# Kernel tuning notes

Measured on AMD Instinct MI355X. Metric: run time of the kernel, lower is better.

## Reference

```python
import jax, jax.numpy as jnp
import numpy as np

L1 = 1e-3  # init kwarg l1
EPS_NORM = 1e-12  # torch F.normalize eps


def _l2_normalize(x):
    # F.normalize(x, p=2, dim=1)
    n = jnp.linalg.norm(x, axis=1, keepdims=True)
    return x / jnp.maximum(n, EPS_NORM)


def _rbf_kernel(x):
    # x: [n, d]
    x2 = jnp.sum(x * x, axis=1, keepdims=True)          # [n,1]
    dist = x2 + x2.T - 2.0 * (x @ x.T)                   # [n,n]
    dist = jnp.maximum(dist, 0.0)
    # torch.median on even-size input returns the LOWER middle element
    flat = jnp.sort(jax.lax.stop_gradient(dist).ravel())
    median_dist = flat[(flat.shape[0] - 1) // 2]
    sigma2 = median_dist + 1e-5
    return jnp.exp(-dist / (2.0 * sigma2))


def _hsic(x, y):
    # x, y: [n, d]. Note: original normalizes in forward AND in hsic; L2
    # normalization is idempotent, so one normalize here is exact.
    x = _l2_normalize(x)
    y = _l2_normalize(y)
    K = _rbf_kernel(x)
    L = _rbf_kernel(y)
    n = K.shape[0]
    # K @ H with H = I - 1/n  ==  K - row_mean(K)
    KH = K - jnp.mean(K, axis=1, keepdims=True)
    LH = L - jnp.mean(L, axis=1, keepdims=True)
    return jnp.sum(KH * LH.T) / float((n - 1) ** 2)


def setup_inputs() -> dict:
    key = jax.random.key(0)
    k1, k2, k3, k4 = jax.random.split(key, 4)
    N, D = 65536, 512     # patches, feature dim
    K_INST, NS = 256, 32  # instances, samples per instance (== max_bg_samples)
    dp = jax.random.normal(k1, (N, D), dtype=jnp.float32)
    gate = jax.random.normal(k2, (N, D), dtype=jnp.float32)
    inst_idx = jax.random.randint(k3, (K_INST, NS), 0, N, dtype=jnp.int64)
    bg_idx = jax.random.randint(k4, (K_INST, NS), 0, N, dtype=jnp.int64)
    return {"dp": dp, "gate": gate, "inst_idx": inst_idx, "bg_idx": bg_idx}


def reference(dp, gate, inst_idx, bg_idx):
    x = dp[inst_idx]   # [K, n, d] per-instance foreground samples
    bg = dp[bg_idx]    # [K, n, d] per-instance background samples
    hs = jax.vmap(_hsic)(x, bg)  # [K]
    return jnp.mean(hs) + L1 * jnp.mean(jnp.abs(gate))
```

## Files before the change

### kernel.cpp

```cpp
#include <hip/hip_runtime.h>
#include <hip/hip_bf16.h>

#define NS 32
#define FD 512
#define K_INST 256
#define CHUNK 256
#define C4 (CHUNK/4)
#define PADF 260
#define PAD4 (PADF/4)
#define MPAD 33
#define HSIC_BLOCKS 512
#define GATE_BLOCKS 512
#define GATE_ITERS 64
#define GATE_N4 (65536*512/4)

__device__ __forceinline__ float wave_reduce_add(float v) {
  for (int off = 32; off; off >>= 1) v += __shfl_down(v, off, 64);
  return v;
}

__global__ __launch_bounds__(256) void fused_kernel(
    const float* __restrict__ dp, const float* __restrict__ gate,
    const int* __restrict__ inst_idx, const int* __restrict__ bg_idx,
    float* __restrict__ ws_gate, float* __restrict__ ws_mats,
    float* __restrict__ ws_means) {

  __shared__ float sX[NS * PADF];
  __shared__ float sD[NS * MPAD];
  __shared__ float sRowM[NS];
  __shared__ float sInv[NS];
  __shared__ float sN2[NS];
  __shared__ int   sIdx[NS];
  __shared__ int   sHist[256];
  __shared__ int   sWaveSum[4];
  __shared__ float sWaveRed[4];
  __shared__ unsigned sPrefix;
  __shared__ int   sWant;

  const int tid  = threadIdx.x;
  const int bid  = blockIdx.x;
  const int lane = tid & 63;
  const int w    = tid >> 6;

  if (bid >= HSIC_BLOCKS) {
    const int gb = bid - HSIC_BLOCKS;
    const float4* g4 = reinterpret_cast<const float4*>(gate);
    float s = 0.f;
    size_t base = (size_t)gb * 256 + tid;
    #pragma unroll 8
    for (int it = 0; it < GATE_ITERS; ++it) {
      float4 v = g4[base + (size_t)it * (GATE_BLOCKS * 256)];
      s += fabsf(v.x) + fabsf(v.y) + fabsf(v.z) + fabsf(v.w);
    }
    s = wave_reduce_add(s);
    if (lane == 0) sWaveRed[w] = s;
    __syncthreads();
    if (tid == 0) ws_gate[gb] = sWaveRed[0] + sWaveRed[1] + sWaveRed[2] + sWaveRed[3];
    return;
  }

  const int k = bid >> 1;
  const int m = bid & 1;
  const int ti = tid >> 4;
  const int tj = tid & 15;
  const float4* sX4 = reinterpret_cast<const float4*>(sX);

  const int* idx = (m == 0 ? inst_idx : bg_idx) + k * NS;
  if (tid < NS) sIdx[tid] = idx[tid];
  __syncthreads();

  float a00 = 0.f, a01 = 0.f, a10 = 0.f, a11 = 0.f;
  for (int ch = 0; ch < 2; ++ch) {
    for (int q = tid; q < NS * C4; q += 256) {
      int r = q >> 6, c = q & 63;
      float4 v = *(reinterpret_cast<const float4*>(dp + (size_t)sIdx[r] * FD + ch * CHUNK) + c);
      *(reinterpret_cast<float4*>(&sX[r * PADF]) + c) = v;
    }
    __syncthreads();
    #pragma unroll 4
    for (int c = 0; c < C4; ++c) {
      float4 x0 = sX4[ti * PAD4 + c];
      float4 x1 = sX4[(ti + 16) * PAD4 + c];
      float4 y0 = sX4[tj * PAD4 + c];
      float4 y1 = sX4[(tj + 16) * PAD4 + c];
      a00 += x0.x*y0.x + x0.y*y0.y + x0.z*y0.z + x0.w*y0.w;
      a01 += x0.x*y1.x + x0.y*y1.y + x0.z*y1.z + x0.w*y1.w;
      a10 += x1.x*y0.x + x1.y*y0.y + x1.z*y0.z + x1.w*y0.w;
      a11 += x1.x*y1.x + x1.y*y1.y + x1.z*y1.z + x1.w*y1.w;
    }
    __syncthreads();
  }

  if (ti == tj) { sN2[ti] = a00; sN2[ti + 16] = a11; }
  __syncthreads();
  if (tid < NS) sInv[tid] = 1.f / fmaxf(sqrtf(sN2[tid]), 1e-12f);
  __syncthreads();

  {
    float i0 = sInv[ti], i1 = sInv[ti + 16], j0 = sInv[tj], j1 = sInv[tj + 16];
    sD[ti * MPAD + tj]               = (ti == tj) ? 0.f : fmaxf(2.f - 2.f * a00 * i0 * j0, 0.f);
    sD[ti * MPAD + (tj + 16)]        = fmaxf(2.f - 2.f * a01 * i0 * j1, 0.f);
    sD[(ti + 16) * MPAD + tj]        = fmaxf(2.f - 2.f * a10 * i1 * j0, 0.f);
    sD[(ti + 16) * MPAD + (tj + 16)] = (ti == tj) ? 0.f : fmaxf(2.f - 2.f * a11 * i1 * j1, 0.f);
  }
  if (tid == 0) { sPrefix = 0u; sWant = (NS * NS - 1) / 2; }
  __syncthreads();

  for (int shift = 24; shift >= 0; shift -= 8) {
    sHist[tid] = 0;
    __syncthreads();
    unsigned pref = sPrefix;
    int want = sWant;
    unsigned hi_mask = (shift == 24) ? 0u : (0xFFFFFFFFu << (shift + 8));
    for (int q = tid; q < NS * NS; q += 256) {
      unsigned u = __float_as_uint(sD[(q >> 5) * MPAD + (q & 31)]);
      if ((u & hi_mask) == pref) atomicAdd(&sHist[(u >> shift) & 255], 1);
    }
    __syncthreads();
    int v = sHist[tid];
    int x = v;
    for (int off = 1; off < 64; off <<= 1) {
      int y = __shfl_up(x, off, 64);
      if (lane >= off) x += y;
    }
    if (lane == 63) sWaveSum[w] = x;
    __syncthreads();
    int add = 0;
    for (int ww = 0; ww < w; ++ww) add += sWaveSum[ww];
    x += add;
    int ex = x - v;
    if (ex <= want && want < ex + v) {
      sPrefix = pref | ((unsigned)tid << shift);
      sWant   = want - ex;
    }
    __syncthreads();
  }
  float sigma2 = __uint_as_float(sPrefix) + 1e-5f;

  float inv2s = -1.f / (2.f * sigma2);
  for (int q = tid; q < NS * NS; q += 256) {
    int i = q >> 5, j = q & 31;
    sD[i * MPAD + j] = expf(sD[i * MPAD + j] * inv2s);
  }
  __syncthreads();

  {
    int r = tid >> 3, g = tid & 7;
    float p = 0.f;
    #pragma unroll
    for (int s = 0; s < 4; ++s) p += sD[r * MPAD + g + 8 * s];
    for (int off = 4; off; off >>= 1) p += __shfl_down(p, off, 8);
    if (g == 0) sRowM[r] = p * (1.f / 32.f);
  }
  __syncthreads();

  float* mat = ws_mats + (size_t)bid * 1024;
  for (int q = tid; q < NS * NS; q += 256)
    mat[q] = sD[(q >> 5) * MPAD + (q & 31)];
  if (tid < NS) ws_means[bid * NS + tid] = sRowM[tid];
}

__global__ __launch_bounds__(256) void contract_kernel(
    const float* __restrict__ ws_mats, const float* __restrict__ ws_means,
    float* __restrict__ ws_hs) {
  __shared__ float sRM[2][NS];
  __shared__ float sWaveRed[4];
  const int k = blockIdx.x;
  const int tid = threadIdx.x, lane = tid & 63, w = tid >> 6;
  const float* Km = ws_mats + (size_t)(k * 2 + 0) * 1024;
  const float* Lm = ws_mats + (size_t)(k * 2 + 1) * 1024;
  if (tid < 64) sRM[tid >> 5][tid & 31] = ws_means[(k * 2 + (tid >> 5)) * NS + (tid & 31)];
  __syncthreads();
  float part = 0.f;
  for (int q = tid; q < NS * NS; q += 256) {
    int i = q >> 5, j = q & 31;
    part += (Km[q] - sRM[0][i]) * (Lm[q] - sRM[1][j]);
  }
  part = wave_reduce_add(part);
  if (lane == 0) sWaveRed[w] = part;
  __syncthreads();
  if (tid == 0)
    ws_hs[k] = (sWaveRed[0] + sWaveRed[1] + sWaveRed[2] + sWaveRed[3]) * (1.f / 961.f);
}

__global__ __launch_bounds__(256) void final_kernel(
    const float* __restrict__ ws_gate, const float* __restrict__ ws_hs,
    float* __restrict__ out) {
  __shared__ float sW[8];
  const int tid = threadIdx.x, lane = tid & 63, wave = tid >> 6;
  float g = 0.f;
  for (int i = tid; i < GATE_BLOCKS; i += 256) g += ws_gate[i];
  g = wave_reduce_add(g);
  if (lane == 0) sW[wave] = g;
  float h = (tid < K_INST) ? ws_hs[tid] : 0.f;
  h = wave_reduce_add(h);
  if (lane == 0) sW[4 + wave] = h;
  __syncthreads();
  if (tid == 0) {
    float gsum = sW[0] + sW[1] + sW[2] + sW[3];
    float hsum = sW[4] + sW[5] + sW[6] + sW[7];
    out[0] = hsum * (1.f / 256.f) + 1e-3f * (gsum / (65536.f * 512.f));
  }
}

extern "C" void kernel_launch(void* const* d_in, const int* in_sizes, int n_in,
                              void* d_out, int out_size, void* d_ws, size_t ws_size,
                              hipStream_t stream) {
  const float* dp   = (const float*)d_in[0];
  const float* gate = (const float*)d_in[1];
  const int*   inst = (const int*)d_in[2];
  const int*   bg   = (const int*)d_in[3];
  float* out = (float*)d_out;
  float* ws  = (float*)d_ws;
  float* ws_gate  = ws;
  float* ws_hs    = ws + 1024;
  float* ws_means = ws + 1024 + 256;
  float* ws_mats  = ws + 1024 + 256 + 512 * 32;

  fused_kernel<<<HSIC_BLOCKS + GATE_BLOCKS, 256, 0, stream>>>(
      dp, gate, inst, bg, ws_gate, ws_mats, ws_means);
  contract_kernel<<<K_INST, 256, 0, stream>>>(ws_mats, ws_means, ws_hs);
  final_kernel<<<1, 256, 0, stream>>>(ws_gate, ws_hs, out);
}
```

Baseline: 45.71 us.

## Keep distance matrix in registers, aggregate histogram atomics, split gate work finer

Each thread now keeps its four distance values in registers instead of writing them to a shared-memory matrix. The norms, exp, row means and output writes are computed directly from those registers, which removes several __syncthreads barriers and LDS round trips. The first radix-select pass aggregates atomics per bin across the wave using ballot, and the histogram is reset inline. The gate reduction is spread over twice as many blocks with half the iterations each, which adds more blocks in exchange for better load balance.

After: 47.68 us. 4.3% more time.

```diff
diff --git a/kernel.cpp b/kernel.cpp
--- a/kernel.cpp
+++ b/kernel.cpp
@@ -8,11 +8,9 @@
 #define C4 (CHUNK/4)
 #define PADF 260
 #define PAD4 (PADF/4)
-#define MPAD 33
 #define HSIC_BLOCKS 512
-#define GATE_BLOCKS 512
-#define GATE_ITERS 64
-#define GATE_N4 (65536*512/4)
+#define GATE_BLOCKS 1024
+#define GATE_ITERS 32
 
 __device__ __forceinline__ float wave_reduce_add(float v) {
   for (int off = 32; off; off >>= 1) v += __shfl_down(v, off, 64);
@@ -26,9 +24,6 @@
     float* __restrict__ ws_means) {
 
   __shared__ float sX[NS * PADF];
-  __shared__ float sD[NS * MPAD];
-  __shared__ float sRowM[NS];
-  __shared__ float sInv[NS];
   __shared__ float sN2[NS];
   __shared__ int   sIdx[NS];
   __shared__ int   sHist[256];
@@ -59,14 +54,16 @@
     return;
   }
 
-  const int k = bid >> 1;
-  const int m = bid & 1;
+  const int k  = bid >> 1;
+  const int m  = bid & 1;
   const int ti = tid >> 4;
   const int tj = tid & 15;
   const float4* sX4 = reinterpret_cast<const float4*>(sX);
 
   const int* idx = (m == 0 ? inst_idx : bg_idx) + k * NS;
   if (tid < NS) sIdx[tid] = idx[tid];
+  sHist[tid] = 0;
+  if (tid == 0) { sPrefix = 0u; sWant = (NS * NS - 1) / 2; }
   __syncthreads();
 
   float a00 = 0.f, a01 = 0.f, a10 = 0.f, a11 = 0.f;
@@ -93,31 +90,44 @@
 
   if (ti == tj) { sN2[ti] = a00; sN2[ti + 16] = a11; }
   __syncthreads();
-  if (tid < NS) sInv[tid] = 1.f / fmaxf(sqrtf(sN2[tid]), 1e-12f);
-  __syncthreads();
-
-  {
-    float i0 = sInv[ti], i1 = sInv[ti + 16], j0 = sInv[tj], j1 = sInv[tj + 16];
-    sD[ti * MPAD + tj]               = (ti == tj) ? 0.f : fmaxf(2.f - 2.f * a00 * i0 * j0, 0.f);
-    sD[ti * MPAD + (tj + 16)]        = fmaxf(2.f - 2.f * a01 * i0 * j1, 0.f);
-    sD[(ti + 16) * MPAD + tj]        = fmaxf(2.f - 2.f * a10 * i1 * j0, 0.f);
-    sD[(ti + 16) * MPAD + (tj + 16)] = (ti == tj) ? 0.f : fmaxf(2.f - 2.f * a11 * i1 * j1, 0.f);
-  }
-  if (tid == 0) { sPrefix = 0u; sWant = (NS * NS - 1) / 2; }
-  __syncthreads();
-
+  float i0 = 1.f / fmaxf(sqrtf(sN2[ti]),      1e-12f);
+  float i1 = 1.f / fmaxf(sqrtf(sN2[ti + 16]), 1e-12f);
+  float j0 = 1.f / fmaxf(sqrtf(sN2[tj]),      1e-12f);
+  float j1 = 1.f / fmaxf(sqrtf(sN2[tj + 16]), 1e-12f);
+
+  float d0 = (ti == tj) ? 0.f : fmaxf(2.f - 2.f * a00 * i0 * j0, 0.f);
+  float d1 = fmaxf(2.f - 2.f * a01 * i0 * j1, 0.f);
+  float d2 = fmaxf(2.f - 2.f * a10 * i1 * j0, 0.f);
+  float d3 = (ti == tj) ? 0.f : fmaxf(2.f - 2.f * a11 * i1 * j1, 0.f);
+  unsigned u[4] = { __float_as_uint(d0), __float_as_uint(d1),
+                    __float_as_uint(d2), __float_as_uint(d3) };
+
+  #pragma unroll 1
   for (int shift = 24; shift >= 0; shift -= 8) {
-    sHist[tid] = 0;
-    __syncthreads();
     unsigned pref = sPrefix;
     int want = sWant;
-    unsigned hi_mask = (shift == 24) ? 0u : (0xFFFFFFFFu << (shift + 8));
-    for (int q = tid; q < NS * NS; q += 256) {
-      unsigned u = __float_as_uint(sD[(q >> 5) * MPAD + (q & 31)]);
-      if ((u & hi_mask) == pref) atomicAdd(&sHist[(u >> shift) & 255], 1);
+    if (shift == 24) {
+      #pragma unroll
+      for (int s = 0; s < 4; ++s) {
+        int bin = (int)(u[s] >> 24);
+        unsigned long long act = __ballot(1);
+        while (act) {
+          int leader = (int)__builtin_ctzll(act);
+          int lbin = __shfl(bin, leader, 64);
+          unsigned long long mm = __ballot(bin == lbin);
+          if (lane == leader) atomicAdd(&sHist[lbin], (int)__popcll(mm));
+          act &= ~mm;
+        }
+      }
+    } else {
+      unsigned hi_mask = 0xFFFFFFFFu << (shift + 8);
+      #pragma unroll
+      for (int s = 0; s < 4; ++s)
+        if ((u[s] & hi_mask) == pref) atomicAdd(&sHist[(u[s] >> shift) & 255], 1);
     }
     __syncthreads();
     int v = sHist[tid];
+    sHist[tid] = 0;
     int x = v;
     for (int off = 1; off < 64; off <<= 1) {
       int y = __shfl_up(x, off, 64);
@@ -138,26 +148,27 @@
   float sigma2 = __uint_as_float(sPrefix) + 1e-5f;
 
   float inv2s = -1.f / (2.f * sigma2);
-  for (int q = tid; q < NS * NS; q += 256) {
-    int i = q >> 5, j = q & 31;
-    sD[i * MPAD + j] = expf(sD[i * MPAD + j] * inv2s);
-  }
-  __syncthreads();
-
-  {
-    int r = tid >> 3, g = tid & 7;
-    float p = 0.f;
-    #pragma unroll
-    for (int s = 0; s < 4; ++s) p += sD[r * MPAD + g + 8 * s];
-    for (int off = 4; off; off >>= 1) p += __shfl_down(p, off, 8);
-    if (g == 0) sRowM[r] = p * (1.f / 32.f);
-  }
-  __syncthreads();
+  float e0 = expf(d0 * inv2s);
+  float e1 = expf(d1 * inv2s);
+  float e2 = expf(d2 * inv2s);
+  float e3 = expf(d3 * inv2s);
 
   float* mat = ws_mats + (size_t)bid * 1024;
-  for (int q = tid; q < NS * NS; q += 256)
-    mat[q] = sD[(q >> 5) * MPAD + (q & 31)];
-  if (tid < NS) ws_means[bid * NS + tid] = sRowM[tid];
+  mat[ti * 32 + tj]             = e0;
+  mat[ti * 32 + tj + 16]        = e1;
+  mat[(ti + 16) * 32 + tj]      = e2;
+  mat[(ti + 16) * 32 + tj + 16] = e3;
+
+  float r0 = e0 + e1;
+  float r1 = e2 + e3;
+  for (int off = 8; off; off >>= 1) {
+    r0 += __shfl_down(r0, off, 16);
+    r1 += __shfl_down(r1, off, 16);
+  }
+  if (tj == 0) {
+    ws_means[bid * NS + ti]      = r0 * (1.f / 32.f);
+    ws_means[bid * NS + ti + 16] = r1 * (1.f / 32.f);
+  }
 }
 
 __global__ __launch_bounds__(256) void contract_kernel(
```
